# Kernel optimization log

Hardware: AMD Instinct MI355X
Metric: run time of the kernel (lower is better)

## Reference

```python
import jax, jax.numpy as jnp
import numpy as np

HEADS = 16


def setup_inputs() -> dict:
    key0 = jax.random.key(0)
    ks = jax.random.split(key0, 12)
    B, S, H = 4, 2048, 1024
    init = lambda k, shape: (jax.random.normal(k, shape, dtype=jnp.float32) * 0.02)
    return {
        "key": jax.random.normal(ks[0], (B, S, H), dtype=jnp.float32),
        "query": jax.random.normal(ks[1], (B, S, H), dtype=jnp.float32),
        "value": jax.random.normal(ks[2], (B, S, H), dtype=jnp.float32),
        "mask": jnp.zeros((B, 1, S, S), dtype=jnp.float32),  # additive mask
        "wq": init(ks[3], (H, H)), "bq": jnp.zeros((H,), jnp.float32),
        "wk": init(ks[4], (H, H)), "bk": jnp.zeros((H,), jnp.float32),
        "wv": init(ks[5], (H, H)), "bv": jnp.zeros((H,), jnp.float32),
        "wo": init(ks[6], (H, H)), "bo": jnp.zeros((H,), jnp.float32),
    }


def reference(key, query, value, mask, wq, bq, wk, bk, wv, bv, wo, bo):
    B, S, H = query.shape
    Hs = H // HEADS
    # Linear projections (torch Linear: x @ W^T + b), split heads -> [B, Hn, S, Hs]
    split = lambda x: x.reshape(B, S, HEADS, Hs).transpose(0, 2, 1, 3)
    q = split(query @ wq.T + bq)
    k = split(key @ wk.T + bk)
    v = split(value @ wv.T + bv)
    scale = 1.0 / jnp.sqrt(jnp.asarray(Hs, q.dtype))
    scores = jnp.einsum("bhqd,bhkd->bhqk", q, k) * scale  # [B, Hn, S, S]
    probs = jax.nn.softmax(scores + mask, axis=-1)  # dropout p=0 -> identity
    ctx = jnp.einsum("bhqk,bhkd->bhqd", probs, v)
    ctx = ctx.transpose(0, 2, 1, 3).reshape(B, S, H)
    return ctx @ wo.T + bo
```

## Files before the change

kernel.cpp:

```cpp
#include <hip/hip_runtime.h>
#include <hip/hip_bf16.h>

typedef __bf16 bf16;
typedef __bf16 bf16x4 __attribute__((ext_vector_type(4)));
typedef __bf16 bf16x8 __attribute__((ext_vector_type(8)));
typedef float f32x4 __attribute__((ext_vector_type(4)));
typedef float f32x16 __attribute__((ext_vector_type(16)));
typedef unsigned u32x4 __attribute__((ext_vector_type(4)));

#define MFMA16(a, b, c) __builtin_amdgcn_mfma_f32_16x16x32_bf16((a), (b), (c), 0, 0, 0)
#define MFMA32(a, b, c) __builtin_amdgcn_mfma_f32_32x32x16_bf16((a), (b), (c), 0, 0, 0)

__device__ __forceinline__ int xcd_swizzle(int bid, int nblk) {
  const int per = nblk >> 3;
  return (bid & 7) * per + (bid >> 3);
}

__device__ __forceinline__ void gload_lds16(const bf16* g, bf16* lds) {
  __builtin_amdgcn_global_load_lds(
      (const __attribute__((address_space(1))) void*)g,
      (__attribute__((address_space(3))) void*)lds, 16, 0, 0);
}

__device__ __forceinline__ unsigned pack2bf(float a, float b) {
  const unsigned short ua = __builtin_bit_cast(unsigned short, (bf16)a);
  const unsigned short ub = __builtin_bit_cast(unsigned short, (bf16)b);
  return (unsigned)ua | ((unsigned)ub << 16);
}

template <typename T> struct StageRegs;
template <> struct StageRegs<float> { float4 lo[4], hi[4]; };
template <> struct StageRegs<bf16> { bf16x8 v[4]; };

template <typename T>
__device__ __forceinline__ void stage_issue(StageRegs<T>& r, const T* base,
                                            int rowstride, int brc, int k0,
                                            int tid) {
#pragma unroll
  for (int i = 0; i < 4; ++i) {
    const int c = i * 256 + tid;
    const int row = c >> 3, lin = c & 7;
    const T* p = base + (size_t)(brc + row) * rowstride + k0 + lin * 8;
    if constexpr (sizeof(T) == 4) {
      r.lo[i] = *reinterpret_cast<const float4*>(p);
      r.hi[i] = *reinterpret_cast<const float4*>(p + 4);
    } else {
      r.v[i] = *reinterpret_cast<const bf16x8*>(p);
    }
  }
}

template <typename T>
__device__ __forceinline__ void stage_write(const StageRegs<T>& r, bf16* sm,
                                            int tid) {
#pragma unroll
  for (int i = 0; i < 4; ++i) {
    const int c = i * 256 + tid;
    const int row = c >> 3, lin = c & 7;
    const int slot = lin ^ (row & 7);
    bf16x8 v;
    if constexpr (sizeof(T) == 4) {
      const float4 a = r.lo[i], b = r.hi[i];
      v[0] = (bf16)a.x; v[1] = (bf16)a.y; v[2] = (bf16)a.z; v[3] = (bf16)a.w;
      v[4] = (bf16)b.x; v[5] = (bf16)b.y; v[6] = (bf16)b.z; v[7] = (bf16)b.w;
    } else {
      v = r.v[i];
    }
    *reinterpret_cast<bf16x8*>(sm + row * 64 + slot * 8) = v;
  }
}

template <typename TA>
__device__ __forceinline__ void gemm_core(const TA* A, const float* W,
                                          int brow, int bcol, int tid, int wm,
                                          int wn, int l15, int l4,
                                          bf16 (*Asm)[8192], bf16 (*Bsm)[8192],
                                          f32x4 (&acc)[4][4]) {
  StageRegs<TA> ra;
  StageRegs<float> rb;
  stage_issue(ra, A, 1024, brow, 0, tid);
  stage_issue(rb, W, 1024, bcol, 0, tid);
  int p = 0;
  for (int t = 0; t < 16; ++t) {
    stage_write(ra, Asm[p], tid);
    stage_write(rb, Bsm[p], tid);
    if (t + 1 < 16) {
      stage_issue(ra, A, 1024, brow, (t + 1) << 6, tid);
      stage_issue(rb, W, 1024, bcol, (t + 1) << 6, tid);
    }
    __syncthreads();
#pragma unroll
    for (int kk = 0; kk < 2; ++kk) {
      bf16x8 af[4], bfr[4];
#pragma unroll
      for (int m = 0; m < 4; ++m) {
        const int row = wm + m * 16 + l15;
        const int slot = (kk * 4 + l4) ^ (row & 7);
        af[m] = *reinterpret_cast<const bf16x8*>(Asm[p] + row * 64 + slot * 8);
      }
#pragma unroll
      for (int n = 0; n < 4; ++n) {
        const int row = wn + n * 16 + l15;
        const int slot = (kk * 4 + l4) ^ (row & 7);
        bfr[n] = *reinterpret_cast<const bf16x8*>(Bsm[p] + row * 64 + slot * 8);
      }
      __builtin_amdgcn_s_setprio(1);
#pragma unroll
      for (int m = 0; m < 4; ++m)
#pragma unroll
        for (int n = 0; n < 4; ++n)
          acc[m][n] = MFMA16(af[m], bfr[n], acc[m][n]);
      __builtin_amdgcn_s_setprio(0);
    }
    __syncthreads();
    p ^= 1;
  }
}

__global__ __launch_bounds__(256, 2) void qkv_gemm_kernel(
    const float* __restrict__ query, const float* __restrict__ key,
    const float* __restrict__ value, const float* __restrict__ wq,
    const float* __restrict__ wk, const float* __restrict__ wv,
    const float* __restrict__ bq, const float* __restrict__ bk,
    const float* __restrict__ bv, bf16* __restrict__ Qws,
    bf16* __restrict__ Kws, bf16* __restrict__ Vt, float qscale) {
  __shared__ bf16 Asm[2][128 * 64];
  __shared__ bf16 Bsm[2][128 * 64];
  const int tid = threadIdx.x;
  const int lane = tid & 63;
  const int wid = tid >> 6;
  const int l15 = lane & 15;
  const int l4 = lane >> 4;
  const int bid = xcd_swizzle(blockIdx.x, 1536);
  const int seg = bid / 512;
  const int inner = bid % 512;
  const int brow = (inner >> 3) << 7;
  const int bcol = (inner & 7) << 7;
  const int wm = (wid >> 1) << 6;
  const int wn = (wid & 1) << 6;

  const float* A = seg == 0 ? query : (seg == 1 ? key : value);
  const float* W = seg == 0 ? wq : (seg == 1 ? wk : wv);
  const float* bias = seg == 0 ? bq : (seg == 1 ? bk : bv);

  f32x4 acc[4][4] = {};
  gemm_core(A, W, brow, bcol, tid, wm, wn, l15, l4, Asm, Bsm, acc);

  const int r0 = brow + wm + l4 * 4;
  const int c0 = bcol + wn + l15;
  if (seg < 2) {
    bf16* C = seg == 0 ? Qws : Kws;
    const float cs = seg == 0 ? qscale : 1.0f;
#pragma unroll
    for (int n = 0; n < 4; ++n) {
      const float bvv = bias[c0 + n * 16];
#pragma unroll
      for (int m = 0; m < 4; ++m)
#pragma unroll
        for (int r = 0; r < 4; ++r)
          C[(size_t)(r0 + m * 16 + r) * 1024 + (c0 + n * 16)] =
              (bf16)((acc[m][n][r] + bvv) * cs);
    }
  } else {
#pragma unroll
    for (int n = 0; n < 4; ++n) {
      const float bvv = bias[c0 + n * 16];
      const int col = c0 + n * 16;
#pragma unroll
      for (int m = 0; m < 4; ++m) {
        const int row = r0 + m * 16;
        const int bq_ = row >> 11;
        const int srow = row & 2047;
        bf16x4 pk4;
#pragma unroll
        for (int r = 0; r < 4; ++r) pk4[r] = (bf16)(acc[m][n][r] + bvv);
        *reinterpret_cast<bf16x4*>(
            &Vt[(size_t)(bq_ * 1024 + col) * 2048 + srow]) = pk4;
      }
    }
  }
}

__global__ __launch_bounds__(256, 2) void out_gemm_kernel(
    const bf16* __restrict__ A, const float* __restrict__ W,
    const float* __restrict__ bias, float* __restrict__ C) {
  __shared__ bf16 Asm[2][128 * 64];
  __shared__ bf16 Bsm[2][128 * 64];
  const int tid = threadIdx.x;
  const int lane = tid & 63;
  const int wid = tid >> 6;
  const int l15 = lane & 15;
  const int l4 = lane >> 4;
  const int bid = xcd_swizzle(blockIdx.x, 512);
  const int brow = (bid >> 3) << 7;
  const int bcol = (bid & 7) << 7;
  const int wm = (wid >> 1) << 6;
  const int wn = (wid & 1) << 6;

  f32x4 acc[4][4] = {};
  gemm_core(A, W, brow, bcol, tid, wm, wn, l15, l4, Asm, Bsm, acc);

  const int r0 = brow + wm + l4 * 4;
  const int c0 = bcol + wn + l15;
#pragma unroll
  for (int n = 0; n < 4; ++n) {
    const float bvv = bias[c0 + n * 16];
#pragma unroll
    for (int m = 0; m < 4; ++m)
#pragma unroll
      for (int r = 0; r < 4; ++r)
        C[(size_t)(r0 + m * 16 + r) * 1024 + (c0 + n * 16)] =
            acc[m][n][r] + bvv;
  }
}

__global__ __launch_bounds__(256, 2) void attn_kernel(
    const bf16* __restrict__ Q, const bf16* __restrict__ Kt,
    const bf16* __restrict__ Vt, const float* __restrict__ mask,
    bf16* __restrict__ ctx) {
  __shared__ bf16 Ksm[3][64 * 64];
  __shared__ bf16 Vsm[3][64 * 64];
  const int lid = xcd_swizzle(blockIdx.x, 1024);
  const int h = lid & 15;
  const int qb = (lid >> 4) & 15;
  const int b = lid >> 8;
  const int tid = threadIdx.x;
  const int lane = tid & 63;
  const int wid = tid >> 6;
  const int l31 = lane & 31;
  const int h5 = lane >> 5;
  const int qbase = qb * 128 + wid * 32;

  bf16x8 qf[4];
#pragma unroll
  for (int c = 0; c < 4; ++c)
    qf[c] = *reinterpret_cast<const bf16x8*>(
        &Q[(size_t)(b * 2048 + qbase + l31) * 1024 + h * 64 + c * 16 + h5 * 8]);

  f32x16 o[2] = {};
  float lrow = 0.f;
  const float LOG2E = 1.44269504088896f;

  const bf16* Kb = Kt + (size_t)b * 2048 * 1024 + h * 64;
  const bf16* Vb = Vt + (size_t)(b * 16 + h) * 64 * 2048;

  const int ca = tid, cb = 256 + tid;
  const int ra_ = ca >> 3, la = (ca & 7) ^ (ra_ & 7);
  const int rb_ = cb >> 3, lb = (cb & 7) ^ (rb_ & 7);
  const int pra = (ra_ & 51) | ((ra_ & 4) << 1) | ((ra_ & 8) >> 1);
  const int prb = (rb_ & 51) | ((rb_ & 4) << 1) | ((rb_ & 8) >> 1);
  const bf16* kga = Kb + (size_t)pra * 1024 + la * 8;
  const bf16* kgb = Kb + (size_t)prb * 1024 + lb * 8;
  const bf16* vga = Vb + (size_t)ra_ * 2048 + la * 8;
  const bf16* vgb = Vb + (size_t)rb_ * 2048 + lb * 8;
  const float* mg = mask + (size_t)b * 2048 * 2048 +
                    (size_t)(qbase + l31) * 2048 + h5 * 8;

  auto stage = [&](int p) {
    gload_lds16(kga, &Ksm[p][tid * 8]);
    gload_lds16(kgb, &Ksm[p][2048 + tid * 8]);
    gload_lds16(vga, &Vsm[p][tid * 8]);
    gload_lds16(vgb, &Vsm[p][2048 + tid * 8]);
    kga += 64 * 1024; kgb += 64 * 1024;
    vga += 64; vgb += 64;
  };
  f32x4 mA[2][4], mB[2][4];
  auto load_mask = [&](f32x4(&mr)[2][4]) {
#pragma unroll
    for (int s = 0; s < 2; ++s)
#pragma unroll
      for (int g = 0; g < 4; ++g)
        mr[s][g] = *reinterpret_cast<const f32x4*>(
            mg + s * 32 + (g >> 1) * 16 + (g & 1) * 4);
    mg += 64;
  };

  auto tile_compute = [&](int p, f32x4(&mr)[2][4]) {
    f32x16 sf[2];
#pragma unroll
    for (int s = 0; s < 2; ++s)
#pragma unroll
      for (int g = 0; g < 4; ++g)
#pragma unroll
        for (int r = 0; r < 4; ++r) sf[s][g * 4 + r] = mr[s][g][r] * LOG2E;

    __builtin_amdgcn_s_setprio(1);
#pragma unroll
    for (int s = 0; s < 2; ++s) {
#pragma unroll
      for (int c = 0; c < 4; ++c) {
        const int row = s * 32 + l31;
        const int slot = (2 * c + h5) ^ (row & 7);
        const bf16x8 kf =
            *reinterpret_cast<const bf16x8*>(&Ksm[p][row * 64 + slot * 8]);
        sf[s] = MFMA32(kf, qf[c], sf[s]);
      }
    }
    __builtin_amdgcn_s_setprio(0);

    unsigned pk[2][4][2];
#pragma unroll
    for (int s = 0; s < 2; ++s) {
#pragma unroll
      for (int g = 0; g < 4; ++g) {
        const float p0 = __builtin_exp2f(sf[s][g * 4 + 0]);
        const float p1 = __builtin_exp2f(sf[s][g * 4 + 1]);
        const float p2 = __builtin_exp2f(sf[s][g * 4 + 2]);
        const float p3 = __builtin_exp2f(sf[s][g * 4 + 3]);
        lrow += (p0 + p1) + (p2 + p3);
        pk[s][g][0] = pack2bf(p0, p1);
        pk[s][g][1] = pack2bf(p2, p3);
      }
    }

    __builtin_amdgcn_s_setprio(1);
#pragma unroll
    for (int c = 0; c < 4; ++c) {
      const int s = c >> 1;
      const int g0 = 2 * (c & 1);
      const u32x4 uu = {pk[s][g0][0], pk[s][g0][1], pk[s][g0 + 1][0],
                        pk[s][g0 + 1][1]};
      const bf16x8 pa = __builtin_bit_cast(bf16x8, uu);
#pragma unroll
      for (int dsub = 0; dsub < 2; ++dsub) {
        const int row = dsub * 32 + l31;
        const int slot = (2 * c + h5) ^ (row & 7);
        const bf16x8 vf =
            *reinterpret_cast<const bf16x8*>(&Vsm[p][row * 64 + slot * 8]);
        o[dsub] = MFMA32(pa, vf, o[dsub]);
      }
    }
    __builtin_amdgcn_s_setprio(0);
  };

  stage(0);
  stage(1);
  load_mask(mA);
  load_mask(mB);

  int p = 0;
  for (int t = 0; t < 32; t += 2) {
    const int p1 = (p + 1 == 3) ? 0 : p + 1;
    const int p2 = (p + 2 >= 3) ? p - 1 : p + 2;
    asm volatile("s_waitcnt vmcnt(20)" ::: "memory");
    __builtin_amdgcn_s_barrier();
    __builtin_amdgcn_sched_barrier(0);
    if (t + 2 < 32) stage(p2);
    tile_compute(p, mA);
    if (t + 2 < 32) load_mask(mA);
    asm volatile("s_waitcnt vmcnt(20)" ::: "memory");
    __builtin_amdgcn_s_barrier();
    __builtin_amdgcn_sched_barrier(0);
    if (t + 3 < 32) stage(p);
    tile_compute(p1, mB);
    if (t + 3 < 32) load_mask(mB);
    p = p2;
  }

  lrow += __shfl_xor(lrow, 32, 64);
  const float linv = __builtin_amdgcn_rcpf(lrow);
#pragma unroll
  for (int reg = 0; reg < 16; ++reg) {
    const int qr = (reg & 3) + 8 * (reg >> 2) + 4 * h5;
    const float li = __shfl(linv, qr, 64);
    const int q = qbase + qr;
#pragma unroll
    for (int dsub = 0; dsub < 2; ++dsub) {
      ctx[(size_t)(b * 2048 + q) * 1024 + h * 64 + dsub * 32 + l31] =
          (bf16)(o[dsub][reg] * li);
    }
  }
}

extern "C" void kernel_launch(void* const* d_in, const int* in_sizes, int n_in,
                              void* d_out, int out_size, void* d_ws,
                              size_t ws_size, hipStream_t stream) {
  const float* key = (const float*)d_in[0];
  const float* query = (const float*)d_in[1];
  const float* value = (const float*)d_in[2];
  const float* mask = (const float*)d_in[3];
  const float* wq = (const float*)d_in[4];
  const float* bq = (const float*)d_in[5];
  const float* wk = (const float*)d_in[6];
  const float* bk = (const float*)d_in[7];
  const float* wv = (const float*)d_in[8];
  const float* bv = (const float*)d_in[9];
  const float* wo = (const float*)d_in[10];
  const float* bo = (const float*)d_in[11];
  float* out = (float*)d_out;

  const size_t NBSH = (size_t)4 * 2048 * 1024;
  bf16* Qws = (bf16*)d_ws;
  bf16* Kws = Qws + NBSH;
  bf16* Vt = Kws + NBSH;

  const dim3 blk(256);
  qkv_gemm_kernel<<<1536, blk, 0, stream>>>(query, key, value, wq, wk, wv, bq,
                                            bk, bv, Qws, Kws, Vt,
                                            0.18033688011112f);
  attn_kernel<<<1024, blk, 0, stream>>>(Qws, Kws, Vt, mask, Qws);
  out_gemm_kernel<<<512, blk, 0, stream>>>(Qws, wo, bo, out);
}
```

Baseline: 295.8 us.

## Pre-convert mask to scaled bf16 and switch attention to double buffering

A new pre-pass kernel converts the fp32 additive mask into bf16, pre-multiplied by log2(e), and stores it in the output buffer as scratch. The attention kernel then reads half as many mask bytes per tile and rebuilds fp32 values with bit shifts instead of multiplies. The attention loop also drops from triple-buffered LDS with fine-grained vmcnt waits to double buffering with __syncthreads, which cuts LDS use and raises the occupancy hint from 2 to 4. The trade-offs are an extra full pass over the mask, weaker load/compute overlap, and rounding of mask values to bf16.

```diff
diff --git a/kernel.cpp b/kernel.cpp
--- a/kernel.cpp
+++ b/kernel.cpp
@@ -214,12 +214,30 @@
   }
 }
 
-__global__ __launch_bounds__(256, 2) void attn_kernel(
+__global__ __launch_bounds__(256) void prep_mask_kernel(
+    const float* __restrict__ mask, bf16* __restrict__ mb) {
+  const float LOG2E = 1.44269504088896f;
+  const size_t tid0 = (size_t)blockIdx.x * 256 + threadIdx.x;
+#pragma unroll
+  for (int c = 0; c < 4; ++c) {
+    const size_t base = (tid0 + (size_t)c * 524288) * 8;
+    const float4 a = *reinterpret_cast<const float4*>(&mask[base]);
+    const float4 b = *reinterpret_cast<const float4*>(&mask[base + 4]);
+    bf16x8 v;
+    v[0] = (bf16)(a.x * LOG2E); v[1] = (bf16)(a.y * LOG2E);
+    v[2] = (bf16)(a.z * LOG2E); v[3] = (bf16)(a.w * LOG2E);
+    v[4] = (bf16)(b.x * LOG2E); v[5] = (bf16)(b.y * LOG2E);
+    v[6] = (bf16)(b.z * LOG2E); v[7] = (bf16)(b.w * LOG2E);
+    *reinterpret_cast<bf16x8*>(&mb[base]) = v;
+  }
+}
+
+__global__ __launch_bounds__(256, 4) void attn_kernel(
     const bf16* __restrict__ Q, const bf16* __restrict__ Kt,
-    const bf16* __restrict__ Vt, const float* __restrict__ mask,
+    const bf16* __restrict__ Vt, const bf16* __restrict__ Mb,
     bf16* __restrict__ ctx) {
-  __shared__ bf16 Ksm[3][64 * 64];
-  __shared__ bf16 Vsm[3][64 * 64];
+  __shared__ bf16 Ksm[2][64 * 64];
+  __shared__ bf16 Vsm[2][64 * 64];
   const int lid = xcd_swizzle(blockIdx.x, 1024);
   const int h = lid & 15;
   const int qb = (lid >> 4) & 15;
@@ -239,7 +257,6 @@
 
   f32x16 o[2] = {};
   float lrow = 0.f;
-  const float LOG2E = 1.44269504088896f;
 
   const bf16* Kb = Kt + (size_t)b * 2048 * 1024 + h * 64;
   const bf16* Vb = Vt + (size_t)(b * 16 + h) * 64 * 2048;
@@ -253,8 +270,8 @@
   const bf16* kgb = Kb + (size_t)prb * 1024 + lb * 8;
   const bf16* vga = Vb + (size_t)ra_ * 2048 + la * 8;
   const bf16* vgb = Vb + (size_t)rb_ * 2048 + lb * 8;
-  const float* mg = mask + (size_t)b * 2048 * 2048 +
-                    (size_t)(qbase + l31) * 2048 + h5 * 8;
+  const bf16* mp = Mb + (size_t)b * 2048 * 2048 +
+                   (size_t)(qbase + l31) * 2048 + h5 * 8;
 
   auto stage = [&](int p) {
     gload_lds16(kga, &Ksm[p][tid * 8]);
@@ -264,25 +281,34 @@
     kga += 64 * 1024; kgb += 64 * 1024;
     vga += 64; vgb += 64;
   };
-  f32x4 mA[2][4], mB[2][4];
-  auto load_mask = [&](f32x4(&mr)[2][4]) {
+  bf16x8 mA[2][2], mB[2][2];
+  auto load_mask = [&](bf16x8(&mr)[2][2]) {
 #pragma unroll
     for (int s = 0; s < 2; ++s)
 #pragma unroll
-      for (int g = 0; g < 4; ++g)
-        mr[s][g] = *reinterpret_cast<const f32x4*>(
-            mg + s * 32 + (g >> 1) * 16 + (g & 1) * 4);
-    mg += 64;
+      for (int run = 0; run < 2; ++run)
+        mr[s][run] =
+            *reinterpret_cast<const bf16x8*>(mp + s * 32 + run * 16);
+    mp += 64;
   };
 
-  auto tile_compute = [&](int p, f32x4(&mr)[2][4]) {
+  auto tile_compute = [&](int p, bf16x8(&mr)[2][2]) {
     f32x16 sf[2];
 #pragma unroll
-    for (int s = 0; s < 2; ++s)
-#pragma unroll
-      for (int g = 0; g < 4; ++g)
-#pragma unroll
-        for (int r = 0; r < 4; ++r) sf[s][g * 4 + r] = mr[s][g][r] * LOG2E;
+    for (int s = 0; s < 2; ++s) {
+      const u32x4 w0 = __builtin_bit_cast(u32x4, mr[s][0]);
+      const u32x4 w1 = __builtin_bit_cast(u32x4, mr[s][1]);
+#pragma unroll
+      for (int g = 0; g < 4; ++g) {
+#pragma unroll
+        for (int r = 0; r < 4; ++r) {
+          const int j = 4 * (g & 1) + r;
+          const unsigned word = (g >> 1) ? w1[j >> 1] : w0[j >> 1];
+          const unsigned bits = (j & 1) ? (word & 0xffff0000u) : (word << 16);
+          sf[s][g * 4 + r] = __builtin_bit_cast(float, bits);
+        }
+      }
+    }
 
     __builtin_amdgcn_s_setprio(1);
 #pragma unroll
@@ -334,27 +360,20 @@
   };
 
   stage(0);
-  stage(1);
   load_mask(mA);
-  load_mask(mB);
-
-  int p = 0;
+  __syncthreads();
+
   for (int t = 0; t < 32; t += 2) {
-    const int p1 = (p + 1 == 3) ? 0 : p + 1;
-    const int p2 = (p + 2 >= 3) ? p - 1 : p + 2;
-    asm volatile("s_waitcnt vmcnt(20)" ::: "memory");
-    __builtin_amdgcn_s_barrier();
-    __builtin_amdgcn_sched_barrier(0);
-    if (t + 2 < 32) stage(p2);
-    tile_compute(p, mA);
-    if (t + 2 < 32) load_mask(mA);
-    asm volatile("s_waitcnt vmcnt(20)" ::: "memory");
-    __builtin_amdgcn_s_barrier();
-    __builtin_amdgcn_sched_barrier(0);
-    if (t + 3 < 32) stage(p);
-    tile_compute(p1, mB);
-    if (t + 3 < 32) load_mask(mB);
-    p = p2;
+    stage(1);
+    load_mask(mB);
+    tile_compute(0, mA);
+    __syncthreads();
+    if (t + 2 < 32) {
+      stage(0);
+      load_mask(mA);
+    }
+    tile_compute(1, mB);
+    __syncthreads();
   }
 
   lrow += __shfl_xor(lrow, 32, 64);
@@ -393,11 +412,13 @@
   bf16* Qws = (bf16*)d_ws;
   bf16* Kws = Qws + NBSH;
   bf16* Vt = Kws + NBSH;
+  bf16* Mb = (bf16*)d_out;
 
   const dim3 blk(256);
+  prep_mask_kernel<<<2048, blk, 0, stream>>>(mask, Mb);
   qkv_gemm_kernel<<<1536, blk, 0, stream>>>(query, key, value, wq, wk, wv, bq,
                                             bk, bv, Qws, Kws, Vt,
                                             0.18033688011112f);
-  attn_kernel<<<1024, blk, 0, stream>>>(Qws, Kws, Vt, mask, Qws);
+  attn_kernel<<<1024, blk, 0, stream>>>(Qws, Kws, Vt, Mb, Qws);
   out_gemm_kernel<<<512, blk, 0, stream>>>(Qws, wo, bo, out);
 }
```

Result: slower. 336.4 us (+13.7%).
